# Performance work log

Measured on AMD Instinct MI355X. Metric: run time of the kernel, lower is better.

## Reference

```python
import math
import jax, jax.numpy as jnp
import numpy as np

B, L, H = 8, 2048, 256


def setup_inputs() -> dict:
    key = jax.random.key(0)
    k1, k2, k3, k4, k5 = jax.random.split(key, 5)
    inputs = jax.random.normal(k1, (B, L, H), dtype=jnp.float32)
    scale = 1.0 / math.sqrt(H)
    Wq = jax.random.normal(k2, (H, H), dtype=jnp.float32) * scale
    Wk = jax.random.normal(k3, (H, H), dtype=jnp.float32) * scale
    Wv = jax.random.normal(k4, (H, H), dtype=jnp.float32) * scale
    lens = jax.random.randint(k5, (B,), L // 2, L + 1)
    lens = lens.at[0].set(L)  # original assumes max(lens) == L
    return {"inputs": inputs, "Wq": Wq, "Wk": Wk, "Wv": Wv, "lens": lens}


def reference(inputs, Wq, Wk, Wv, lens):
    # nn.Linear(bias=False): y = x @ W.T
    Q = jnp.einsum('blh,oh->blo', inputs, Wq)
    K = jnp.einsum('blh,oh->blo', inputs, Wk)
    V = jnp.einsum('blh,oh->blo', inputs, Wv)
    d = Q.shape[-1]
    alpha = jnp.einsum('bqd,bkd->bqk', Q, K) / math.sqrt(d)  # [B, L, L]
    # key-padding mask: [B, 1, L] broadcast over query dim (matches expand)
    mask = (jnp.arange(L)[None, :] < lens[:, None])[:, None, :]
    NEG = jnp.float32(-2.0 ** 31)
    alpha = jnp.where(mask, alpha, NEG)
    alpha = jax.nn.softmax(alpha, axis=2)
    out = jnp.einsum('bqk,bkd->bqd', alpha, V)
    return out
```

## Files before the change

### kernel.cpp

```cpp
#include <hip/hip_runtime.h>

#define BB 8
#define LL 2048
#define DD 256

typedef _Float16 half8 __attribute__((ext_vector_type(8)));
typedef float floatx4 __attribute__((ext_vector_type(4)));
typedef unsigned short ushort8 __attribute__((ext_vector_type(8)));

__device__ inline unsigned short f2h(float f) {
  _Float16 h = (_Float16)f;
  return __builtin_bit_cast(unsigned short, h);
}

__global__ __launch_bounds__(256) void wcvt(
    const float* __restrict__ Wq, const float* __restrict__ Wk,
    const float* __restrict__ Wv, unsigned short* __restrict__ Wh) {
  const int bm = blockIdx.x >> 5;
  const float* src = (bm == 0) ? Wq : (bm == 1) ? Wk : Wv;
  const int off = (blockIdx.x & 31) * 2048 + threadIdx.x * 8;
  float4 a = *(const float4*)(src + off);
  float4 b = *(const float4*)(src + off + 4);
  ushort8 u = {f2h(a.x), f2h(a.y), f2h(a.z), f2h(a.w),
               f2h(b.x), f2h(b.y), f2h(b.z), f2h(b.w)};
  *(ushort8*)(Wh + bm * 65536 + off) = u;
}

__global__ __launch_bounds__(256) void proj(
    const float* __restrict__ x, const unsigned short* __restrict__ Wh,
    unsigned short* __restrict__ Qb, unsigned short* __restrict__ Kb,
    unsigned short* __restrict__ VT) {
  const int t = threadIdx.x;
  const int wave = t >> 6, lane = t & 63, quad = lane >> 4, m16 = lane & 15;
  const int l0g = blockIdx.x * 32;
  const int b = l0g >> 11, lb = l0g & 2047;

  half8 xf[2][8];
  for (int mt = 0; mt < 2; ++mt) {
    const float* xp = x + (size_t)(l0g + mt * 16 + m16) * DD + quad * 8;
    for (int kb = 0; kb < 8; ++kb) {
      float4 a = *(const float4*)(xp + kb * 32);
      float4 c = *(const float4*)(xp + kb * 32 + 4);
      ushort8 u = {f2h(a.x), f2h(a.y), f2h(a.z), f2h(a.w),
                   f2h(c.x), f2h(c.y), f2h(c.z), f2h(c.w)};
      xf[mt][kb] = __builtin_bit_cast(half8, u);
    }
  }

  for (int j = 0; j < 12; ++j) {
    const int nt = wave * 12 + j;
    const int mat = nt >> 4, ot = nt & 15;
    const unsigned short* wp =
        Wh + mat * 65536 + (ot * 16 + m16) * DD + quad * 8;
    floatx4 acc[2] = {{0, 0, 0, 0}, {0, 0, 0, 0}};
    if (mat < 2) {
      for (int kb = 0; kb < 8; ++kb) {
        half8 wf = __builtin_bit_cast(half8, *(const ushort8*)(wp + kb * 32));
        acc[0] = __builtin_amdgcn_mfma_f32_16x16x32_f16(xf[0][kb], wf, acc[0], 0, 0, 0);
        acc[1] = __builtin_amdgcn_mfma_f32_16x16x32_f16(xf[1][kb], wf, acc[1], 0, 0, 0);
      }
      unsigned short* Out = mat ? Kb : Qb;
      for (int mt = 0; mt < 2; ++mt)
        for (int r = 0; r < 4; ++r)
          Out[(size_t)(l0g + mt * 16 + quad * 4 + r) * DD + ot * 16 + m16] =
              f2h(acc[mt][r]);
    } else {
      for (int kb = 0; kb < 8; ++kb) {
        half8 wf = __builtin_bit_cast(half8, *(const ushort8*)(wp + kb * 32));
        acc[0] = __builtin_amdgcn_mfma_f32_16x16x32_f16(wf, xf[0][kb], acc[0], 0, 0, 0);
        acc[1] = __builtin_amdgcn_mfma_f32_16x16x32_f16(wf, xf[1][kb], acc[1], 0, 0, 0);
      }
      for (int mt = 0; mt < 2; ++mt)
        for (int r = 0; r < 4; ++r)
          VT[((size_t)(b * DD + ot * 16 + quad * 4 + r)) * LL + lb + mt * 16 +
             m16] = f2h(acc[mt][r]);
    }
  }
}

__global__ __launch_bounds__(512, 2) void attn(
    const unsigned short* __restrict__ Qb, const unsigned short* __restrict__ Kb,
    const unsigned short* __restrict__ VT, const int* __restrict__ lens,
    float* __restrict__ out) {
  __shared__ __attribute__((aligned(16))) unsigned char smem[149504];
  const int t = threadIdx.x;
  const int wave = t >> 6, lane = t & 63, quad = lane >> 4, m16 = lane & 15;
  const int grp = wave >> 2, qw = wave & 3, tgl = t & 255;
  unsigned short* Ks = (unsigned short*)(smem + grp * 32768);
  unsigned short* Vs = (unsigned short*)(smem + 65536 + grp * 32768);
  unsigned short* Pw = (unsigned short*)(smem + 131072 + wave * 2304);

  const int b = blockIdx.y;
  const int q0 = blockIdx.x * 64;
  const int len = lens[b];
  const size_t baseQK = (size_t)b * LL * DD;
  const size_t baseVT = (size_t)b * DD * LL;

  half8 qf[8];
  {
    const unsigned short* qrow =
        Qb + baseQK + (size_t)(q0 + qw * 16 + m16) * DD + quad * 8;
    for (int kb = 0; kb < 8; ++kb)
      qf[kb] = __builtin_bit_cast(half8, *(const ushort8*)(qrow + kb * 32));
  }

  floatx4 O[16];
  for (int i = 0; i < 16; ++i) O[i] = (floatx4){0, 0, 0, 0};
  float mrow[4] = {-1e30f, -1e30f, -1e30f, -1e30f};
  float lrow[4] = {0.f, 0.f, 0.f, 0.f};

  ushort8 kreg[8], vreg[8];
  const unsigned short* kbase = Kb + baseQK;
  const unsigned short* vbase = VT + baseVT;

#define LOAD_TILES(KV0)                                                      \
  {                                                                          \
    const unsigned short* kp = kbase + (size_t)(KV0)*DD;                     \
    for (int c = 0; c < 8; ++c)                                              \
      kreg[c] = *(const ushort8*)(kp + (tgl + c * 256) * 8);                 \
    for (int c = 0; c < 8; ++c) {                                            \
      int ch = tgl + c * 256;                                                \
      vreg[c] = *(const ushort8*)(vbase + (size_t)(ch >> 3) * LL + (KV0) +   \
                                  (ch & 7) * 8);                             \
    }                                                                        \
  }

  const int T = (len + 127) >> 7;
  LOAD_TILES(grp * 64);

  for (int it = 0; it < T; ++it) {
    const int kv0 = it * 128 + grp * 64;
    __syncthreads();
    for (int c = 0; c < 8; ++c) {
      int ch = tgl + c * 256, row = ch >> 5, cc = ch & 31;
      *(ushort8*)&Ks[row * 256 + (cc ^ (row & 7)) * 8] = kreg[c];
    }
    for (int c = 0; c < 8; ++c) {
      int ch = tgl + c * 256, d = ch >> 3, cc = ch & 7;
      *(ushort8*)&Vs[d * 64 + (cc ^ (d & 7)) * 8] = vreg[c];
    }
    __syncthreads();
    if (it + 1 < T) LOAD_TILES(kv0 + 128);

    if (kv0 < len) {
      floatx4 s[4];
      for (int n = 0; n < 4; ++n) s[n] = (floatx4){0, 0, 0, 0};
      for (int kb = 0; kb < 8; ++kb)
        for (int n = 0; n < 4; ++n) {
          half8 kf = __builtin_bit_cast(
              half8, *(const ushort8*)&Ks[(n * 16 + m16) * 256 +
                                          (((kb * 4 + quad) ^ (m16 & 7)) * 8)]);
          s[n] = __builtin_amdgcn_mfma_f32_16x16x32_f16(qf[kb], kf, s[n], 0, 0, 0);
        }
      float sv[4][4];
      for (int n = 0; n < 4; ++n) {
        bool valid = (kv0 + n * 16 + m16) < len;
        for (int r = 0; r < 4; ++r)
          sv[n][r] = valid ? s[n][r] * 0.0625f : -1e30f;
      }
      float al[4];
      for (int r = 0; r < 4; ++r) {
        float v = fmaxf(fmaxf(sv[0][r], sv[1][r]), fmaxf(sv[2][r], sv[3][r]));
        v = fmaxf(v, __shfl_xor(v, 1));
        v = fmaxf(v, __shfl_xor(v, 2));
        v = fmaxf(v, __shfl_xor(v, 4));
        v = fmaxf(v, __shfl_xor(v, 8));
        float mn = fmaxf(mrow[r], v);
        al[r] = __expf(mrow[r] - mn);
        mrow[r] = mn;
        float sum = 0.f;
        for (int n = 0; n < 4; ++n) {
          float p = __expf(sv[n][r] - mn);
          Pw[(quad * 4 + r) * 72 + n * 16 + m16] = f2h(p);
          sum += p;
        }
        sum += __shfl_xor(sum, 1);
        sum += __shfl_xor(sum, 2);
        sum += __shfl_xor(sum, 4);
        sum += __shfl_xor(sum, 8);
        lrow[r] = lrow[r] * al[r] + sum;
      }
      for (int i = 0; i < 16; ++i)
        for (int r = 0; r < 4; ++r) O[i][r] *= al[r];
      half8 pf0 = __builtin_bit_cast(half8,
                                     *(const ushort8*)&Pw[m16 * 72 + quad * 8]);
      half8 pf1 = __builtin_bit_cast(
          half8, *(const ushort8*)&Pw[m16 * 72 + 32 + quad * 8]);
      for (int nb = 0; nb < 16; ++nb) {
        half8 vf0 = __builtin_bit_cast(
            half8, *(const ushort8*)&Vs[(nb * 16 + m16) * 64 +
                                        ((quad ^ (m16 & 7)) * 8)]);
        O[nb] = __builtin_amdgcn_mfma_f32_16x16x32_f16(pf0, vf0, O[nb], 0, 0, 0);
        half8 vf1 = __builtin_bit_cast(
            half8, *(const ushort8*)&Vs[(nb * 16 + m16) * 64 +
                                        (((4 + quad) ^ (m16 & 7)) * 8)]);
        O[nb] = __builtin_amdgcn_mfma_f32_16x16x32_f16(pf1, vf1, O[nb], 0, 0, 0);
      }
    }
  }
#undef LOAD_TILES

  __syncthreads();
  float* Om = (float*)(smem) + qw * 4112;
  float* ml = (float*)(smem + 65792) + qw * 32;
  if (grp == 1) {
    for (int nb = 0; nb < 16; ++nb)
      for (int r = 0; r < 4; ++r)
        Om[(quad * 4 + r) * 257 + nb * 16 + m16] = O[nb][r];
    if (m16 == 0)
      for (int r = 0; r < 4; ++r) {
        ml[(quad * 4 + r) * 2] = mrow[r];
        ml[(quad * 4 + r) * 2 + 1] = lrow[r];
      }
  }
  __syncthreads();
  if (grp == 0) {
    float a[4], bf[4], inv[4];
    for (int r = 0; r < 4; ++r) {
      float mB = ml[(quad * 4 + r) * 2];
      float lB = ml[(quad * 4 + r) * 2 + 1];
      float m = fmaxf(mrow[r], mB);
      a[r] = __expf(mrow[r] - m);
      bf[r] = __expf(mB - m);
      inv[r] = 1.f / (lrow[r] * a[r] + lB * bf[r]);
    }
    for (int nb = 0; nb < 16; ++nb)
      for (int r = 0; r < 4; ++r) {
        float ob = Om[(quad * 4 + r) * 257 + nb * 16 + m16];
        out[baseQK + (size_t)(q0 + qw * 16 + quad * 4 + r) * DD + nb * 16 +
            m16] = (O[nb][r] * a[r] + ob * bf[r]) * inv[r];
      }
  }
}

extern "C" void kernel_launch(void* const* d_in, const int* in_sizes, int n_in,
                              void* d_out, int out_size, void* d_ws, size_t ws_size,
                              hipStream_t stream) {
  const float* x = (const float*)d_in[0];
  const float* Wq = (const float*)d_in[1];
  const float* Wk = (const float*)d_in[2];
  const float* Wv = (const float*)d_in[3];
  const int* lens = (const int*)d_in[4];
  unsigned short* Qb = (unsigned short*)d_ws;
  unsigned short* Kb = Qb + (size_t)BB * LL * DD;
  unsigned short* VT = Kb + (size_t)BB * LL * DD;
  unsigned short* Wh = VT + (size_t)BB * LL * DD;
  float* out = (float*)d_out;

  wcvt<<<96, 256, 0, stream>>>(Wq, Wk, Wv, Wh);
  proj<<<512, 256, 0, stream>>>(x, Wh, Qb, Kb, VT);
  attn<<<dim3(32, 8), 512, 0, stream>>>(Qb, Kb, VT, lens, out);
}
```

Baseline: 193.7 us.

## Stage projection outputs through LDS for coalesced stores; reorder attn grid and add priorities

The projection kernel now writes each matrix's MFMA results into a shared-memory tile and then stores them to global memory as 16-byte vectors, replacing scattered 2-byte stores. This matters most for the transposed V output. The attention grid is swapped so batch varies fastest, which interleaves blocks with different sequence lengths across the GPU. The attention loop also raises wave priority around the MFMA sections and adds compiler memory barriers after the prefetch loads. The tradeoffs are extra syncthreads and LDS use in the projection kernel, and a change in how attention blocks are scheduled.

```diff
diff --git a/kernel.cpp b/kernel.cpp
--- a/kernel.cpp
+++ b/kernel.cpp
@@ -30,6 +30,7 @@
     const float* __restrict__ x, const unsigned short* __restrict__ Wh,
     unsigned short* __restrict__ Qb, unsigned short* __restrict__ Kb,
     unsigned short* __restrict__ VT) {
+  __shared__ __attribute__((aligned(16))) unsigned short tile[10240];
   const int t = threadIdx.x;
   const int wave = t >> 6, lane = t & 63, quad = lane >> 4, m16 = lane & 15;
   const int l0g = blockIdx.x * 32;
@@ -47,34 +48,57 @@
     }
   }
 
-  for (int j = 0; j < 12; ++j) {
-    const int nt = wave * 12 + j;
-    const int mat = nt >> 4, ot = nt & 15;
-    const unsigned short* wp =
-        Wh + mat * 65536 + (ot * 16 + m16) * DD + quad * 8;
-    floatx4 acc[2] = {{0, 0, 0, 0}, {0, 0, 0, 0}};
+  for (int mat = 0; mat < 3; ++mat) {
+    for (int j = 0; j < 4; ++j) {
+      const int ot = wave * 4 + j;
+      const unsigned short* wp =
+          Wh + mat * 65536 + (ot * 16 + m16) * DD + quad * 8;
+      floatx4 acc[2] = {{0, 0, 0, 0}, {0, 0, 0, 0}};
+      if (mat < 2) {
+        for (int kb = 0; kb < 8; ++kb) {
+          half8 wf =
+              __builtin_bit_cast(half8, *(const ushort8*)(wp + kb * 32));
+          acc[0] = __builtin_amdgcn_mfma_f32_16x16x32_f16(xf[0][kb], wf,
+                                                          acc[0], 0, 0, 0);
+          acc[1] = __builtin_amdgcn_mfma_f32_16x16x32_f16(xf[1][kb], wf,
+                                                          acc[1], 0, 0, 0);
+        }
+        for (int mt = 0; mt < 2; ++mt)
+          for (int r = 0; r < 4; ++r)
+            tile[(mt * 16 + quad * 4 + r) * 264 + ot * 16 + m16] =
+                f2h(acc[mt][r]);
+      } else {
+        for (int kb = 0; kb < 8; ++kb) {
+          half8 wf =
+              __builtin_bit_cast(half8, *(const ushort8*)(wp + kb * 32));
+          acc[0] = __builtin_amdgcn_mfma_f32_16x16x32_f16(wf, xf[0][kb],
+                                                          acc[0], 0, 0, 0);
+          acc[1] = __builtin_amdgcn_mfma_f32_16x16x32_f16(wf, xf[1][kb],
+                                                          acc[1], 0, 0, 0);
+        }
+        for (int mt = 0; mt < 2; ++mt)
+          for (int r = 0; r < 4; ++r)
+            tile[(ot * 16 + quad * 4 + r) * 40 + mt * 16 + m16] =
+                f2h(acc[mt][r]);
+      }
+    }
+    __syncthreads();
     if (mat < 2) {
-      for (int kb = 0; kb < 8; ++kb) {
-        half8 wf = __builtin_bit_cast(half8, *(const ushort8*)(wp + kb * 32));
-        acc[0] = __builtin_amdgcn_mfma_f32_16x16x32_f16(xf[0][kb], wf, acc[0], 0, 0, 0);
-        acc[1] = __builtin_amdgcn_mfma_f32_16x16x32_f16(xf[1][kb], wf, acc[1], 0, 0, 0);
-      }
       unsigned short* Out = mat ? Kb : Qb;
-      for (int mt = 0; mt < 2; ++mt)
-        for (int r = 0; r < 4; ++r)
-          Out[(size_t)(l0g + mt * 16 + quad * 4 + r) * DD + ot * 16 + m16] =
-              f2h(acc[mt][r]);
+      const int row = t >> 3, c0 = (t & 7) * 8;
+      for (int i = 0; i < 4; ++i) {
+        ushort8 v = *(const ushort8*)&tile[row * 264 + c0 + i * 64];
+        *(ushort8*)(Out + (size_t)(l0g + row) * DD + c0 + i * 64) = v;
+      }
     } else {
-      for (int kb = 0; kb < 8; ++kb) {
-        half8 wf = __builtin_bit_cast(half8, *(const ushort8*)(wp + kb * 32));
-        acc[0] = __builtin_amdgcn_mfma_f32_16x16x32_f16(wf, xf[0][kb], acc[0], 0, 0, 0);
-        acc[1] = __builtin_amdgcn_mfma_f32_16x16x32_f16(wf, xf[1][kb], acc[1], 0, 0, 0);
-      }
-      for (int mt = 0; mt < 2; ++mt)
-        for (int r = 0; r < 4; ++r)
-          VT[((size_t)(b * DD + ot * 16 + quad * 4 + r)) * LL + lb + mt * 16 +
-             m16] = f2h(acc[mt][r]);
-    }
+      const int dd = t >> 2, lc = (t & 3) * 8;
+      for (int p = 0; p < 4; ++p) {
+        const int d = p * 64 + dd;
+        ushort8 v = *(const ushort8*)&tile[d * 40 + lc];
+        *(ushort8*)(VT + ((size_t)(b * DD + d)) * LL + lb + lc) = v;
+      }
+    }
+    __syncthreads();
   }
 }
 
@@ -90,8 +114,8 @@
   unsigned short* Vs = (unsigned short*)(smem + 65536 + grp * 32768);
   unsigned short* Pw = (unsigned short*)(smem + 131072 + wave * 2304);
 
-  const int b = blockIdx.y;
-  const int q0 = blockIdx.x * 64;
+  const int b = blockIdx.x;
+  const int q0 = blockIdx.y * 64;
   const int len = lens[b];
   const size_t baseQK = (size_t)b * LL * DD;
   const size_t baseVT = (size_t)b * DD * LL;
@@ -127,6 +151,7 @@
 
   const int T = (len + 127) >> 7;
   LOAD_TILES(grp * 64);
+  asm volatile("" ::: "memory");
 
   for (int it = 0; it < T; ++it) {
     const int kv0 = it * 128 + grp * 64;
@@ -140,11 +165,15 @@
       *(ushort8*)&Vs[d * 64 + (cc ^ (d & 7)) * 8] = vreg[c];
     }
     __syncthreads();
-    if (it + 1 < T) LOAD_TILES(kv0 + 128);
+    if (it + 1 < T) {
+      LOAD_TILES(kv0 + 128);
+      asm volatile("" ::: "memory");
+    }
 
     if (kv0 < len) {
       floatx4 s[4];
       for (int n = 0; n < 4; ++n) s[n] = (floatx4){0, 0, 0, 0};
+      __builtin_amdgcn_s_setprio(1);
       for (int kb = 0; kb < 8; ++kb)
         for (int n = 0; n < 4; ++n) {
           half8 kf = __builtin_bit_cast(
@@ -152,6 +181,7 @@
                                           (((kb * 4 + quad) ^ (m16 & 7)) * 8)]);
           s[n] = __builtin_amdgcn_mfma_f32_16x16x32_f16(qf[kb], kf, s[n], 0, 0, 0);
         }
+      __builtin_amdgcn_s_setprio(0);
       float sv[4][4];
       for (int n = 0; n < 4; ++n) {
         bool valid = (kv0 + n * 16 + m16) < len;
@@ -186,6 +216,7 @@
                                      *(const ushort8*)&Pw[m16 * 72 + quad * 8]);
       half8 pf1 = __builtin_bit_cast(
           half8, *(const ushort8*)&Pw[m16 * 72 + 32 + quad * 8]);
+      __builtin_amdgcn_s_setprio(1);
       for (int nb = 0; nb < 16; ++nb) {
         half8 vf0 = __builtin_bit_cast(
             half8, *(const ushort8*)&Vs[(nb * 16 + m16) * 64 +
@@ -196,6 +227,7 @@
                                         (((4 + quad) ^ (m16 & 7)) * 8)]);
         O[nb] = __builtin_amdgcn_mfma_f32_16x16x32_f16(pf1, vf1, O[nb], 0, 0, 0);
       }
+      __builtin_amdgcn_s_setprio(0);
     }
   }
 #undef LOAD_TILES
@@ -249,5 +281,5 @@
 
   wcvt<<<96, 256, 0, stream>>>(Wq, Wk, Wv, Wh);
   proj<<<512, 256, 0, stream>>>(x, Wh, Qb, Kb, VT);
-  attn<<<dim3(32, 8), 512, 0, stream>>>(Qb, Kb, VT, lens, out);
-}
+  attn<<<dim3(8, 32), 512, 0, stream>>>(Qb, Kb, VT, lens, out);
+}
```

Result: faster. 182.6 us (-5.7%).
